# Kernel tuning notes

Hardware: AMD Instinct MI355X
Metric: run time of the kernel (lower is better)

Reference implementation:

```python
import jax, jax.numpy as jnp
import numpy as np

K = 20
BN_SCALE = 1.0 / np.sqrt(1.0 + 1e-5)  # BN at init: running_mean=0, running_var=1


def _graph_feature(x, k):
    # x: (B, N, C) point features -> (B, N, k, 2C) edge features
    sq = jnp.sum(x * x, axis=-1)  # (B, N)
    # negative squared distance: larger == closer (matches torch topk on -dist)
    d = 2.0 * jnp.einsum('bnc,bmc->bnm', x, x) - sq[:, :, None] - sq[:, None, :]
    idx = jax.lax.top_k(d, k)[1]  # (B, N, k), self included as nearest
    nbr = jax.vmap(lambda pts, i: pts[i])(x, idx)  # (B, N, k, C) gather
    ctr = jnp.broadcast_to(x[:, :, None, :], nbr.shape)
    return jnp.concatenate([nbr - ctr, ctr], axis=-1)


def _edge_conv(e, W, g, b):
    # 1x1 Conv2d (no bias) + BatchNorm(init stats) + LeakyReLU(0.2) + max over k
    y = jnp.einsum('bnkc,oc->bnko', e, W)
    y = jax.nn.leaky_relu(y * (g * BN_SCALE) + b, 0.2)
    return jnp.max(y, axis=2)  # (B, N, O)


def setup_inputs() -> dict:
    key = jax.random.key(0)
    ks = jax.random.split(key, 12)
    B, N = 4, 1024
    dims_in = [6, 128, 256, 512]
    dims_out = [64, 128, 256, 512]
    inp = {'x': jax.random.normal(ks[0], (B, N, 3), dtype=jnp.float32)}
    for i, (ci, co) in enumerate(zip(dims_in, dims_out), start=1):
        inp[f'W{i}'] = jax.random.normal(ks[i], (co, ci), dtype=jnp.float32) * (1.0 / np.sqrt(ci))
        inp[f'g{i}'] = jnp.ones((co,), dtype=jnp.float32)
        inp[f'b{i}'] = jnp.zeros((co,), dtype=jnp.float32)
    inp['W5'] = jax.random.normal(ks[5], (512, 960), dtype=jnp.float32) * (1.0 / np.sqrt(960.0))
    inp['g5'] = jnp.ones((512,), dtype=jnp.float32)
    inp['b5'] = jnp.zeros((512,), dtype=jnp.float32)
    inp['We'] = jax.random.normal(ks[6], (256, 512), dtype=jnp.float32) * (1.0 / np.sqrt(512.0))
    return inp


def reference(x, W1, g1, b1, W2, g2, b2, W3, g3, b3, W4, g4, b4, W5, g5, b5, We):
    x1 = _edge_conv(_graph_feature(x, K), W1, g1, b1)   # (B, N, 64)
    x2 = _edge_conv(_graph_feature(x1, K), W2, g2, b2)  # (B, N, 128)
    x3 = _edge_conv(_graph_feature(x2, K), W3, g3, b3)  # (B, N, 256)
    x4 = _edge_conv(_graph_feature(x3, K), W4, g4, b4)  # (B, N, 512)
    xc = jnp.concatenate([x1, x2, x3, x4], axis=-1)     # (B, N, 960)
    y = jnp.einsum('bnc,oc->bno', xc, W5)               # conv5 (1x1 Conv1d)
    y = jax.nn.leaky_relu(y * (g5 * BN_SCALE) + b5, 0.2)
    feat = jnp.max(y, axis=1)                           # (B, 512) global max-pool
    return feat @ We.T                                  # (B, num_features)
```

## Files before the change

kernel.cpp:

```cpp
#include <hip/hip_runtime.h>
#include <hip/hip_bf16.h>
#include <math.h>

typedef __hip_bfloat16 bf16;
typedef __bf16 v8bf __attribute__((ext_vector_type(8)));
typedef float v4f __attribute__((ext_vector_type(4)));

#define BN_SCALE 0.9999950000374997f
#define NPTS 1024
#define NB 4
#define CH5 ((size_t)4 * 1024 * 512)

__device__ __forceinline__ float b2f(bf16 v) { return __bfloat162float(v); }
__device__ __forceinline__ bf16 f2b(float v) { return __float2bfloat16(v); }
__device__ __forceinline__ float ldw(const void* p, size_t i, int isf) {
    return isf ? ((const float*)p)[i] : b2f(((const bf16*)p)[i]);
}
__device__ __forceinline__ unsigned ordf(float f) {
    unsigned u = __float_as_uint(f);
    return (u & 0x80000000u) ? ~u : (u | 0x80000000u);
}
__device__ __forceinline__ float iordf(unsigned u) {
    return (u & 0x80000000u) ? __uint_as_float(u ^ 0x80000000u) : __uint_as_float(~u);
}

__device__ __forceinline__ int detect_isf(const void* xraw, int* cnt) {
    const unsigned short* u = (const unsigned short*)xraw;
    int t = threadIdx.x, c = 0;
    for (int i = t; i < 512; i += 256) {
        unsigned short v = u[i];
        int e = (v >> 7) & 0xFF;
        int m = v & 0x7F;
        if (e == 0xFF || e >= 141 || (e == 0 && m != 0)) c++;
    }
    cnt[t] = c;
    __syncthreads();
    for (int off = 128; off > 0; off >>= 1) {
        if (t < off) cnt[t] += cnt[t + off];
        __syncthreads();
    }
    int isf = (cnt[0] > 30) ? 1 : 0;
    __syncthreads();
    return isf;
}

__global__ void k_prep(const void* __restrict__ W1, const void* __restrict__ W2,
                       const void* __restrict__ W3, const void* __restrict__ W4,
                       const void* __restrict__ W5, const void* __restrict__ x,
                       bf16* __restrict__ Whi, bf16* __restrict__ Wlo,
                       bf16* __restrict__ xph, bf16* __restrict__ xpl, float* __restrict__ sq,
                       int* __restrict__ flag, unsigned* __restrict__ pooledU) {
    __shared__ int cnt[256];
    int isf = detect_isf(x, cnt);
    if (blockIdx.x == 0) {
        if (threadIdx.x == 0) *flag = isf;
        for (int i = threadIdx.x; i < 2048; i += 256) pooledU[i] = 0u;
    }
    int idx = blockIdx.x * 256 + threadIdx.x;
    if (idx < 839680) {
        const void* src; int C, O, Kpad, two, local;
        if (idx < 4096)        { src = W1; C = 3;   O = 64;  Kpad = 32;  two = 1; local = idx; }
        else if (idx < 20480)  { src = W2; C = 64;  O = 128; Kpad = 64;  two = 1; local = idx - 4096; }
        else if (idx < 86016)  { src = W3; C = 128; O = 256; Kpad = 128; two = 1; local = idx - 20480; }
        else if (idx < 348160) { src = W4; C = 256; O = 512; Kpad = 256; two = 1; local = idx - 86016; }
        else                   { src = W5; C = 960; O = 512; Kpad = 960; two = 0; local = idx - 348160; }
        int r = local / Kpad, c = local % Kpad;
        float wv = 0.f;
        if (c < C) {
            size_t off;
            if (two) off = (r < O) ? (size_t)r * 2 * C + c : (size_t)(r - O) * 2 * C + C + c;
            else     off = (size_t)r * C + c;
            wv = ldw(src, off, isf);
        }
        bf16 h = f2b(wv);
        Whi[idx] = h;
        Wlo[idx] = f2b(wv - b2f(h));
    } else if (idx < 843776) {
        int p = idx - 839680;
        int z = p >> 10, n = p & 1023;
        bf16* ph = xph + (size_t)z * NPTS * 32;
        bf16* pl = xpl + (size_t)z * NPTS * 32;
        float s = 0.f;
        for (int c = 0; c < 32; c++) {
            float v = (c < 3) ? ldw(x, (size_t)z * NPTS * 3 + n * 3 + c, isf) : 0.f;
            bf16 h = f2b(v);
            ph[n * 32 + c] = h;
            pl[n * 32 + c] = f2b(v - b2f(h));
            s += v * v;
        }
        sq[z * NPTS + n] = s;
    }
}

__device__ __forceinline__ int lidx(int plane, int row) {
    return ((((plane << 7) | row)) ^ (plane << 1)) << 3;
}
__device__ __forceinline__ void fill128(bf16* dst, const bf16* src, int ld) {
    int t = threadIdx.x;
    int r = t >> 2, kq = t & 3;
    *(float4*)(dst + lidx(kq, r))      = *(const float4*)(src + (size_t)r * ld + kq * 8);
    *(float4*)(dst + lidx(kq, r + 64)) = *(const float4*)(src + (size_t)(r + 64) * ld + kq * 8);
}
__device__ __forceinline__ v8bf ldf(const bf16* tile, int sub, int l) {
    return *(const v8bf*)(tile + lidx(l >> 4, sub * 16 + (l & 15)));
}

__global__ __launch_bounds__(256) void k_layer_a(const bf16* __restrict__ Xhi, const bf16* __restrict__ Xlo,
                                                 int ld, int Kpad, size_t xstride,
                                                 const bf16* __restrict__ Whi, const bf16* __restrict__ Wlo,
                                                 int O, const float* __restrict__ sqg,
                                                 float* __restrict__ Dg, float* __restrict__ Pg,
                                                 const int* __restrict__ flag) {
    int i = blockIdx.x;
    int z = (i >> 1) & 3;
    int bi = ((i >> 3) << 1) | (i & 1);
    const bf16* Xh = Xhi + (size_t)z * xstride;
    const bf16* Xl = Xlo + (size_t)z * xstride;
    __shared__ alignas(16) bf16 Ah[4096], Al[4096], Bh[4096], Bl[4096];
    int w = threadIdx.x >> 6, l = threadIdx.x & 63;
    int wr = w >> 1, wc = w & 1;
    int quad = l >> 4, col = l & 15;
    v4f zero = {0.f, 0.f, 0.f, 0.f};
    v4f acc[4][4] = {{zero, zero, zero, zero}, {zero, zero, zero, zero},
                     {zero, zero, zero, zero}, {zero, zero, zero, zero}};

    if (bi < 36) {
        int bx = 0;
        while ((((bx + 1) * (bx + 2)) >> 1) <= bi) bx++;
        int by = bi - ((bx * (bx + 1)) >> 1);
        const float* sq = sqg + z * NPTS;
        float* D = Dg + (size_t)z * NPTS * NPTS;
        int n0 = by * 128, m0 = bx * 128;
        for (int k0 = 0; k0 < Kpad; k0 += 32) {
            __syncthreads();
            fill128(Ah, Xh + (size_t)n0 * ld + k0, ld);
            fill128(Bh, Xh + (size_t)m0 * ld + k0, ld);
            fill128(Al, Xl + (size_t)n0 * ld + k0, ld);
            fill128(Bl, Xl + (size_t)m0 * ld + k0, ld);
            __syncthreads();
            v8bf ah[4], al[4];
#pragma unroll
            for (int mi = 0; mi < 4; mi++) {
                ah[mi] = ldf(Ah, wr * 4 + mi, l);
                al[mi] = ldf(Al, wr * 4 + mi, l);
            }
#pragma unroll
            for (int ni = 0; ni < 4; ni++) {
                v8bf bh = ldf(Bh, wc * 4 + ni, l);
                v8bf bl = ldf(Bl, wc * 4 + ni, l);
#pragma unroll
                for (int mi = 0; mi < 4; mi++) {
                    acc[mi][ni] = __builtin_amdgcn_mfma_f32_16x16x32_bf16(ah[mi], bh, acc[mi][ni], 0, 0, 0);
                    acc[mi][ni] = __builtin_amdgcn_mfma_f32_16x16x32_bf16(ah[mi], bl, acc[mi][ni], 0, 0, 0);
                    acc[mi][ni] = __builtin_amdgcn_mfma_f32_16x16x32_bf16(al[mi], bh, acc[mi][ni], 0, 0, 0);
                }
            }
        }
        int rb = n0 + wr * 64 + quad * 4;
        int cb = m0 + wc * 64 + col;
        float sm[4];
#pragma unroll
        for (int ni = 0; ni < 4; ni++) sm[ni] = sq[cb + ni * 16];
#pragma unroll
        for (int mi = 0; mi < 4; mi++) {
#pragma unroll
            for (int r = 0; r < 4; r++) {
                int row = rb + mi * 16 + r;
                float sn = sq[row];
#pragma unroll
                for (int ni = 0; ni < 4; ni++) {
                    float d = 2.f * acc[mi][ni][r] - sn - sm[ni];
                    int c = cb + ni * 16;
                    D[(size_t)row * NPTS + c] = d;
                    if (bx != by) D[(size_t)c * NPTS + row] = d;
                }
            }
        }
    } else {
        int isf = *flag;
        int nCol = (2 * O) >> 7;
        int s = bi - 36;
        int n0 = (s % nCol) * 128;
        int m0 = (s / nCol) * 128;
        int N2 = 2 * O;
        float* P = Pg + (size_t)z * NPTS * N2;
        for (int k0 = 0; k0 < Kpad; k0 += 32) {
            __syncthreads();
            fill128(Ah, Xh + (size_t)m0 * ld + k0, ld);
            fill128(Al, Xl + (size_t)m0 * ld + k0, ld);
            fill128(Bh, Whi + (size_t)n0 * Kpad + k0, Kpad);
            if (isf) fill128(Bl, Wlo + (size_t)n0 * Kpad + k0, Kpad);
            __syncthreads();
            v8bf ah[4], al[4];
#pragma unroll
            for (int mi = 0; mi < 4; mi++) {
                ah[mi] = ldf(Ah, wr * 4 + mi, l);
                al[mi] = ldf(Al, wr * 4 + mi, l);
            }
#pragma unroll
            for (int ni = 0; ni < 4; ni++) {
                v8bf bh = ldf(Bh, wc * 4 + ni, l);
#pragma unroll
                for (int mi = 0; mi < 4; mi++) {
                    acc[mi][ni] = __builtin_amdgcn_mfma_f32_16x16x32_bf16(ah[mi], bh, acc[mi][ni], 0, 0, 0);
                    acc[mi][ni] = __builtin_amdgcn_mfma_f32_16x16x32_bf16(al[mi], bh, acc[mi][ni], 0, 0, 0);
                }
                if (isf) {
                    v8bf bl = ldf(Bl, wc * 4 + ni, l);
#pragma unroll
                    for (int mi = 0; mi < 4; mi++)
                        acc[mi][ni] = __builtin_amdgcn_mfma_f32_16x16x32_bf16(ah[mi], bl, acc[mi][ni], 0, 0, 0);
                }
            }
        }
        int rb = m0 + wr * 64 + quad * 4;
        int cb = n0 + wc * 64 + col;
#pragma unroll
        for (int mi = 0; mi < 4; mi++)
#pragma unroll
            for (int r = 0; r < 4; r++) {
                int row = rb + mi * 16 + r;
#pragma unroll
                for (int ni = 0; ni < 4; ni++)
                    P[(size_t)row * N2 + cb + ni * 16] = acc[mi][ni][r];
            }
    }
}

template<int PAT>
__device__ __forceinline__ void swz_step(float& bv, int& bi) {
    float ov = __int_as_float(__builtin_amdgcn_ds_swizzle(__float_as_int(bv), PAT));
    int   oi = __builtin_amdgcn_ds_swizzle(bi, PAT);
    if (ov > bv || (ov == bv && oi < bi)) { bv = ov; bi = oi; }
}
__device__ __forceinline__ void shfl_step(float& bv, int& bi, int mask) {
    float ov = __shfl_xor(bv, mask);
    int   oi = __shfl_xor(bi, mask);
    if (ov > bv || (ov == bv && oi < bi)) { bv = ov; bi = oi; }
}
#define PICK(va, ja, vb, jb, vo, jo) { bool t_ = (vb) > (va); vo = t_ ? (vb) : (va); jo = t_ ? (jb) : (ja); }

#define GATHER_BODY(o, scl, bb, doSq) do { \
    float tv = Pn[O + (o)] - Pn[(o)]; \
    float mx = -__builtin_inff(), mn = __builtin_inff(); \
    _Pragma("unroll") \
    for (int j = 0; j < 20; j++) { \
        float vv = P[offj[j] + (o)]; \
        mx = fmaxf(mx, vv); \
        mn = fminf(mn, vv); \
    } \
    float base = ((scl) >= 0.f ? mx : mn) + tv; \
    float accv = base * (scl) + (bb); \
    accv = accv > 0.f ? accv : 0.2f * accv; \
    bf16 hi = f2b(accv); \
    bf16 lo = f2b(accv - b2f(hi)); \
    xhOut[(size_t)z * NPTS * 960 + (size_t)n * 960 + (o)] = hi; \
    xlOut[(size_t)z * NPTS * 960 + (size_t)n * 960 + (o)] = lo; \
    if (doSq) { \
        float xv = b2f(hi) + b2f(lo); \
        float s2 = xv * xv; \
        _Pragma("unroll") \
        for (int off = 32; off > 0; off >>= 1) s2 += __shfl_down(s2, off); \
        if (l == 0) sqP[r][(o) >> 6] = s2; \
    } \
} while (0)

__global__ __launch_bounds__(256) void k_layer_b(const float* __restrict__ Dg, const float* __restrict__ Pg,
                                                 const void* __restrict__ g, const void* __restrict__ bias,
                                                 int O, bf16* __restrict__ xhOut, bf16* __restrict__ xlOut,
                                                 float* __restrict__ sqOut, int writeSq,
                                                 const int* __restrict__ flag) {
    __shared__ int ids[4][20];
    __shared__ float sqP[4][8];
    int isf = *flag;
    int i = blockIdx.x;
    int z = (i >> 1) & 3;
    int local = ((i >> 3) << 1) | (i & 1);
    int tid = threadIdx.x;
    int wq = tid >> 6, l = tid & 63;
    int row = local * 4 + wq;

    {
        const float* Dr = Dg + (size_t)z * NPTS * NPTS + (size_t)row * NPTS;
        float v[16];
#pragma unroll
        for (int jj = 0; jj < 4; jj++) {
            float4 f4 = *(const float4*)(Dr + jj * 256 + l * 4);
            v[jj * 4 + 0] = f4.x; v[jj * 4 + 1] = f4.y;
            v[jj * 4 + 2] = f4.z; v[jj * 4 + 3] = f4.w;
        }
        float bmv[4]; int bmj[4];
#pragma unroll
        for (int gg = 0; gg < 4; gg++) {
            float a0, a1; int j0, j1;
            PICK(v[4 * gg + 0], 4 * gg + 0, v[4 * gg + 1], 4 * gg + 1, a0, j0);
            PICK(v[4 * gg + 2], 4 * gg + 2, v[4 * gg + 3], 4 * gg + 3, a1, j1);
            PICK(a0, j0, a1, j1, bmv[gg], bmj[gg]);
        }
        for (int s = 0; s < 20; s++) {
            float t0, t1, bv; int s0, s1, bj;
            PICK(bmv[0], bmj[0], bmv[1], bmj[1], t0, s0);
            PICK(bmv[2], bmj[2], bmv[3], bmj[3], t1, s1);
            PICK(t0, s0, t1, s1, bv, bj);
            int bi = (bj >> 2) * 256 + l * 4 + (bj & 3);
            swz_step<0x041F>(bv, bi);
            swz_step<0x081F>(bv, bi);
            swz_step<0x101F>(bv, bi);
            swz_step<0x201F>(bv, bi);
            swz_step<0x401F>(bv, bi);
            shfl_step(bv, bi, 32);
            if (l == 0) ids[wq][s] = bi;
            if (((bi >> 2) & 63) == l) {
                int ej = (bi >> 8) * 4 + (bi & 3);
                int eg = ej >> 2, ek = ej & 3;
#pragma unroll
                for (int gg = 0; gg < 4; gg++) if (gg == eg) {
#pragma unroll
                    for (int kk = 0; kk < 4; kk++)
                        if (kk == ek) v[4 * gg + kk] = -__builtin_inff();
                    float a0, a1; int j0, j1;
                    PICK(v[4 * gg + 0], 4 * gg + 0, v[4 * gg + 1], 4 * gg + 1, a0, j0);
                    PICK(v[4 * gg + 2], 4 * gg + 2, v[4 * gg + 3], 4 * gg + 3, a1, j1);
                    PICK(a0, j0, a1, j1, bmv[gg], bmj[gg]);
                }
            }
        }
    }
    __syncthreads();

    int N2 = 2 * O;
    const float* P = Pg + (size_t)z * NPTS * N2;
    int o0 = tid, o1 = tid + 256;
    int has0 = (o0 < O), has1 = (o1 < O);
    float scl0 = 0.f, bb0 = 0.f, scl1 = 0.f, bb1 = 0.f;
    if (has0) { scl0 = ldw(g, o0, isf) * BN_SCALE; bb0 = ldw(bias, o0, isf); }
    if (has1) { scl1 = ldw(g, o1, isf) * BN_SCALE; bb1 = ldw(bias, o1, isf); }
#pragma unroll
    for (int r = 0; r < 4; r++) {
        int offj[20];
#pragma unroll
        for (int j = 0; j < 20; j++)
            offj[j] = __builtin_amdgcn_readfirstlane(ids[r][j]) * N2;
        int n = local * 4 + r;
        const float* Pn = P + (size_t)n * N2;
        if (has0) GATHER_BODY(o0, scl0, bb0, writeSq);
        if (has1) GATHER_BODY(o1, scl1, bb1, 0);
    }
    if (writeSq) {
        __syncthreads();
        if (tid < 4) {
            int nc = O >> 6;
            float tot = 0.f;
            for (int c = 0; c < nc; c++) tot += sqP[tid][c];
            sqOut[z * NPTS + local * 4 + tid] = tot;
        }
    }
}

__global__ __launch_bounds__(256) void k_conv5(const bf16* __restrict__ Xhi, const bf16* __restrict__ Xlo,
                                               const bf16* __restrict__ Whi, const bf16* __restrict__ Wlo,
                                               float* __restrict__ P5,
                                               const int* __restrict__ flag) {
    int isf = *flag;
    int i = blockIdx.x;
    int z = (i >> 1) & 3;
    int rest = ((i >> 3) << 1) | (i & 1);
    int ks = rest >> 5;
    int tile = rest & 31;
    int m0 = (tile >> 2) * 128, o0 = (tile & 3) * 128;
    const bf16* Xh = Xhi + (size_t)z * NPTS * 960;
    const bf16* Xl = Xlo + (size_t)z * NPTS * 960;
    __shared__ alignas(16) bf16 Ah[4096], Al[4096], Bh[4096], Bl[4096];
    int w = threadIdx.x >> 6, l = threadIdx.x & 63;
    int wr = w >> 1, wc = w & 1;
    int quad = l >> 4, col = l & 15;
    v4f zero = {0.f, 0.f, 0.f, 0.f};
    v4f acc[4][4] = {{zero, zero, zero, zero}, {zero, zero, zero, zero},
                     {zero, zero, zero, zero}, {zero, zero, zero, zero}};
    int kbeg = ks * 160, kend = kbeg + 160;
    for (int k0 = kbeg; k0 < kend; k0 += 32) {
        __syncthreads();
        fill128(Ah, Xh + (size_t)m0 * 960 + k0, 960);
        fill128(Al, Xl + (size_t)m0 * 960 + k0, 960);
        fill128(Bh, Whi + (size_t)o0 * 960 + k0, 960);
        if (isf) fill128(Bl, Wlo + (size_t)o0 * 960 + k0, 960);
        __syncthreads();
        v8bf ah[4], al[4];
#pragma unroll
        for (int mi = 0; mi < 4; mi++) {
            ah[mi] = ldf(Ah, wr * 4 + mi, l);
            al[mi] = ldf(Al, wr * 4 + mi, l);
        }
#pragma unroll
        for (int ni = 0; ni < 4; ni++) {
            v8bf bh = ldf(Bh, wc * 4 + ni, l);
#pragma unroll
            for (int mi = 0; mi < 4; mi++) {
                acc[mi][ni] = __builtin_amdgcn_mfma_f32_16x16x32_bf16(ah[mi], bh, acc[mi][ni], 0, 0, 0);
                acc[mi][ni] = __builtin_amdgcn_mfma_f32_16x16x32_bf16(al[mi], bh, acc[mi][ni], 0, 0, 0);
            }
            if (isf) {
                v8bf bl = ldf(Bl, wc * 4 + ni, l);
#pragma unroll
                for (int mi = 0; mi < 4; mi++)
                    acc[mi][ni] = __builtin_amdgcn_mfma_f32_16x16x32_bf16(ah[mi], bl, acc[mi][ni], 0, 0, 0);
            }
        }
    }
    float* Pw = P5 + (size_t)ks * CH5 + (size_t)z * NPTS * 512;
    int rb = m0 + wr * 64 + quad * 4;
    int cb = o0 + wc * 64 + col;
#pragma unroll
    for (int mi = 0; mi < 4; mi++)
#pragma unroll
        for (int r = 0; r < 4; r++) {
            int row = rb + mi * 16 + r;
#pragma unroll
            for (int ni = 0; ni < 4; ni++)
                Pw[(size_t)row * 512 + cb + ni * 16] = acc[mi][ni][r];
        }
}

__global__ __launch_bounds__(256) void k_pool5(const float* __restrict__ P5,
                                               const void* __restrict__ g, const void* __restrict__ bias,
                                               unsigned* __restrict__ pooledU,
                                               const int* __restrict__ flag) {
    __shared__ float red2[128];
    int isf = *flag;
    int i = blockIdx.x;
    int z = (i >> 1) & 3;
    int rest = ((i >> 3) << 1) | (i & 1);
    int oc = (rest & 3) * 128, mc = (rest >> 2) * 32;
    int t = threadIdx.x;
    int c = t & 127, h = t >> 7;
    int o = oc + c;
    float scl = ldw(g, o, isf) * BN_SCALE;
    float bb = ldw(bias, o, isf);
    const float* p0 = P5 + (size_t)z * NPTS * 512 + (size_t)(mc + h * 16) * 512 + o;
    float ym = -__builtin_inff();
    for (int r = 0; r < 16; r++) {
        const float* p = p0 + (size_t)r * 512;
        float s = p[0];
#pragma unroll
        for (int ks = 1; ks < 6; ks++) s += p[(size_t)ks * CH5];
        float v = s * scl + bb;
        v = v > 0.f ? v : 0.2f * v;
        ym = fmaxf(ym, v);
    }
    if (h == 1) red2[c] = ym;
    __syncthreads();
    if (h == 0) {
        float m = fmaxf(ym, red2[c]);
        atomicMax(&pooledU[z * 512 + o], ordf(m));
    }
}

__global__ void k_final(const unsigned* __restrict__ pooledU, const void* __restrict__ We,
                        void* __restrict__ out, const int* __restrict__ flag) {
    __shared__ float p[512];
    int isf = *flag;
    int b = blockIdx.x >> 2, fb = blockIdx.x & 3;
    int t = threadIdx.x, w = t >> 6, l = t & 63;
    for (int i = t; i < 512; i += 256) p[i] = iordf(pooledU[b * 512 + i]);
    __syncthreads();
    for (int it = 0; it < 16; it++) {
        int f = fb * 64 + w * 16 + it;
        float s = 0.f;
        size_t base = (size_t)f * 512 + l * 8;
#pragma unroll
        for (int j = 0; j < 8; j++) s += p[l * 8 + j] * ldw(We, base + j, isf);
#pragma unroll
        for (int off = 32; off > 0; off >>= 1) s += __shfl_down(s, off);
        if (l == 0) {
            if (isf) ((float*)out)[b * 256 + f] = s;
            else     ((bf16*)out)[b * 256 + f] = f2b(s);
        }
    }
}

extern "C" void kernel_launch(void* const* d_in, const int* in_sizes, int n_in,
                              void* d_out, int out_size, void* d_ws, size_t ws_size,
                              hipStream_t stream) {
    const void* x  = d_in[0];
    const void* Wl[4] = { d_in[1], d_in[4], d_in[7], d_in[10] };
    const void* gl[4] = { d_in[2], d_in[5], d_in[8], d_in[11] };
    const void* bl[4] = { d_in[3], d_in[6], d_in[9], d_in[12] };
    const void* W5 = d_in[13];
    const void* g5 = d_in[14];
    const void* b5 = d_in[15];
    const void* We = d_in[16];

    char* base = (char*)d_ws;
    bf16*     xc_hi   = (bf16*)(base);
    bf16*     xc_lo   = (bf16*)(base + 7864320);
    bf16*     xpadh   = (bf16*)(base + 15728640);
    bf16*     xpadl   = (bf16*)(base + 15990784);
    float*    Dbuf    = (float*)(base + 16252928);
    float*    Pbuf    = (float*)(base + 33030144);
    bf16*     Whi     = (bf16*)(base + 49807360);
    bf16*     Wlo     = (bf16*)(base + 51486720);
    unsigned* pooledU = (unsigned*)(base + 53493760);
    float*    sq      = (float*)(base + 53501952);
    int*      flag    = (int*)(base + 53518336);
    float*    P5      = (float*)(base + 53520384);

    const int Kpad[4]   = { 32, 64, 128, 256 };
    const int Os[4]     = { 64, 128, 256, 512 };
    const int Woff[5]   = { 0, 4096, 20480, 86016, 348160 };
    const int colIn[4]  = { 0, 0, 64, 192 };
    const int colOut[4] = { 0, 64, 192, 448 };

    k_prep<<<3296, 256, 0, stream>>>(Wl[0], Wl[1], Wl[2], Wl[3], W5, x,
                                     Whi, Wlo, xpadh, xpadl, sq, flag, pooledU);

    for (int l = 0; l < 4; l++) {
        int O = Os[l];
        int nCol = (2 * O) >> 7;
        int nBlk = 36 + 8 * nCol;
        const bf16* Xh = (l == 0) ? xpadh : (xc_hi + colIn[l]);
        const bf16* Xl = (l == 0) ? xpadl : (xc_lo + colIn[l]);
        int ld = (l == 0) ? 32 : 960;
        size_t xstr = (l == 0) ? (size_t)NPTS * 32 : (size_t)NPTS * 960;
        k_layer_a<<<nBlk * NB, 256, 0, stream>>>(
            Xh, Xl, ld, Kpad[l], xstr, Whi + Woff[l], Wlo + Woff[l], O, sq, Dbuf, Pbuf, flag);
        k_layer_b<<<NPTS * NB / 4, 256, 0, stream>>>(
            Dbuf, Pbuf, gl[l], bl[l], O, xc_hi + colOut[l], xc_lo + colOut[l], sq, l < 3, flag);
    }
    k_conv5<<<768, 256, 0, stream>>>(xc_hi, xc_lo, Whi + Woff[4], Wlo + Woff[4], P5, flag);
    k_pool5<<<512, 256, 0, stream>>>(P5, g5, b5, pooledU, flag);
    k_final<<<16, 256, 0, stream>>>(pooledU, We, d_out, flag);
}
```

Baseline: 321.0 us.

## Double-buffer LDS tiles with register prefetch in layer GEMM kernel

Converts the k-loop of both branches of k_layer_a (distance GEMM and weight projection GEMM) into a software pipeline. The next K-slice is loaded from global memory into registers before the MFMA work on the current slice, then written to a second LDS buffer afterwards, leaving one barrier per iteration instead of two. This aims to hide global load latency behind the matrix math, at the cost of doubling LDS use (64 KB) and holding extra registers for the staged data, which may reduce occupancy.

```diff
diff --git a/kernel.cpp b/kernel.cpp
--- a/kernel.cpp
+++ b/kernel.cpp
@@ -95,6 +95,19 @@
 __device__ __forceinline__ int lidx(int plane, int row) {
     return ((((plane << 7) | row)) ^ (plane << 1)) << 3;
 }
+struct St2 { float4 a, b; };
+__device__ __forceinline__ St2 ldStage(const bf16* src, int ld) {
+    int t = threadIdx.x; int r = t >> 2, kq = t & 3;
+    St2 s;
+    s.a = *(const float4*)(src + (size_t)r * ld + kq * 8);
+    s.b = *(const float4*)(src + (size_t)(r + 64) * ld + kq * 8);
+    return s;
+}
+__device__ __forceinline__ void stStage(bf16* dst, const St2& s) {
+    int t = threadIdx.x; int r = t >> 2, kq = t & 3;
+    *(float4*)(dst + lidx(kq, r)) = s.a;
+    *(float4*)(dst + lidx(kq, r + 64)) = s.b;
+}
 __device__ __forceinline__ void fill128(bf16* dst, const bf16* src, int ld) {
     int t = threadIdx.x;
     int r = t >> 2, kq = t & 3;
@@ -116,7 +129,7 @@
     int bi = ((i >> 3) << 1) | (i & 1);
     const bf16* Xh = Xhi + (size_t)z * xstride;
     const bf16* Xl = Xlo + (size_t)z * xstride;
-    __shared__ alignas(16) bf16 Ah[4096], Al[4096], Bh[4096], Bl[4096];
+    __shared__ alignas(16) bf16 Ah[2][4096], Al[2][4096], Bh[2][4096], Bl[2][4096];
     int w = threadIdx.x >> 6, l = threadIdx.x & 63;
     int wr = w >> 1, wc = w & 1;
     int quad = l >> 4, col = l & 15;
@@ -131,23 +144,34 @@
         const float* sq = sqg + z * NPTS;
         float* D = Dg + (size_t)z * NPTS * NPTS;
         int n0 = by * 128, m0 = bx * 128;
+        const bf16* pAn = Xh + (size_t)n0 * ld;
+        const bf16* pAm = Xh + (size_t)m0 * ld;
+        const bf16* pLn = Xl + (size_t)n0 * ld;
+        const bf16* pLm = Xl + (size_t)m0 * ld;
+        St2 sA = ldStage(pAn, ld), sB = ldStage(pAm, ld);
+        St2 sC = ldStage(pLn, ld), sD = ldStage(pLm, ld);
+        stStage(Ah[0], sA); stStage(Bh[0], sB);
+        stStage(Al[0], sC); stStage(Bl[0], sD);
+        __syncthreads();
+        int cur = 0;
         for (int k0 = 0; k0 < Kpad; k0 += 32) {
-            __syncthreads();
-            fill128(Ah, Xh + (size_t)n0 * ld + k0, ld);
-            fill128(Bh, Xh + (size_t)m0 * ld + k0, ld);
-            fill128(Al, Xl + (size_t)n0 * ld + k0, ld);
-            fill128(Bl, Xl + (size_t)m0 * ld + k0, ld);
-            __syncthreads();
+            bool more = (k0 + 32 < Kpad);
+            if (more) {
+                sA = ldStage(pAn + k0 + 32, ld);
+                sB = ldStage(pAm + k0 + 32, ld);
+                sC = ldStage(pLn + k0 + 32, ld);
+                sD = ldStage(pLm + k0 + 32, ld);
+            }
             v8bf ah[4], al[4];
 #pragma unroll
             for (int mi = 0; mi < 4; mi++) {
-                ah[mi] = ldf(Ah, wr * 4 + mi, l);
-                al[mi] = ldf(Al, wr * 4 + mi, l);
+                ah[mi] = ldf(Ah[cur], wr * 4 + mi, l);
+                al[mi] = ldf(Al[cur], wr * 4 + mi, l);
             }
 #pragma unroll
             for (int ni = 0; ni < 4; ni++) {
-                v8bf bh = ldf(Bh, wc * 4 + ni, l);
-                v8bf bl = ldf(Bl, wc * 4 + ni, l);
+                v8bf bh = ldf(Bh[cur], wc * 4 + ni, l);
+                v8bf bl = ldf(Bl[cur], wc * 4 + ni, l);
 #pragma unroll
                 for (int mi = 0; mi < 4; mi++) {
                     acc[mi][ni] = __builtin_amdgcn_mfma_f32_16x16x32_bf16(ah[mi], bh, acc[mi][ni], 0, 0, 0);
@@ -155,6 +179,12 @@
                     acc[mi][ni] = __builtin_amdgcn_mfma_f32_16x16x32_bf16(al[mi], bh, acc[mi][ni], 0, 0, 0);
                 }
             }
+            if (more) {
+                stStage(Ah[cur ^ 1], sA); stStage(Bh[cur ^ 1], sB);
+                stStage(Al[cur ^ 1], sC); stStage(Bl[cur ^ 1], sD);
+            }
+            __syncthreads();
+            cur ^= 1;
         }
         int rb = n0 + wr * 64 + quad * 4;
         int cb = m0 + wc * 64 + col;
@@ -184,34 +214,53 @@
         int m0 = (s / nCol) * 128;
         int N2 = 2 * O;
         float* P = Pg + (size_t)z * NPTS * N2;
+        const bf16* pXh = Xh + (size_t)m0 * ld;
+        const bf16* pXl = Xl + (size_t)m0 * ld;
+        const bf16* pWh = Whi + (size_t)n0 * Kpad;
+        const bf16* pWl = Wlo + (size_t)n0 * Kpad;
+        St2 sA = ldStage(pXh, ld), sC = ldStage(pXl, ld);
+        St2 sB = ldStage(pWh, Kpad), sD;
+        if (isf) sD = ldStage(pWl, Kpad);
+        stStage(Ah[0], sA); stStage(Al[0], sC); stStage(Bh[0], sB);
+        if (isf) stStage(Bl[0], sD);
+        __syncthreads();
+        int cur = 0;
         for (int k0 = 0; k0 < Kpad; k0 += 32) {
-            __syncthreads();
-            fill128(Ah, Xh + (size_t)m0 * ld + k0, ld);
-            fill128(Al, Xl + (size_t)m0 * ld + k0, ld);
-            fill128(Bh, Whi + (size_t)n0 * Kpad + k0, Kpad);
-            if (isf) fill128(Bl, Wlo + (size_t)n0 * Kpad + k0, Kpad);
-            __syncthreads();
+            bool more = (k0 + 32 < Kpad);
+            if (more) {
+                sA = ldStage(pXh + k0 + 32, ld);
+                sC = ldStage(pXl + k0 + 32, ld);
+                sB = ldStage(pWh + k0 + 32, Kpad);
+                if (isf) sD = ldStage(pWl + k0 + 32, Kpad);
+            }
             v8bf ah[4], al[4];
 #pragma unroll
             for (int mi = 0; mi < 4; mi++) {
-                ah[mi] = ldf(Ah, wr * 4 + mi, l);
-                al[mi] = ldf(Al, wr * 4 + mi, l);
+                ah[mi] = ldf(Ah[cur], wr * 4 + mi, l);
+                al[mi] = ldf(Al[cur], wr * 4 + mi, l);
             }
 #pragma unroll
             for (int ni = 0; ni < 4; ni++) {
-                v8bf bh = ldf(Bh, wc * 4 + ni, l);
+                v8bf bh = ldf(Bh[cur], wc * 4 + ni, l);
 #pragma unroll
                 for (int mi = 0; mi < 4; mi++) {
                     acc[mi][ni] = __builtin_amdgcn_mfma_f32_16x16x32_bf16(ah[mi], bh, acc[mi][ni], 0, 0, 0);
                     acc[mi][ni] = __builtin_amdgcn_mfma_f32_16x16x32_bf16(al[mi], bh, acc[mi][ni], 0, 0, 0);
                 }
                 if (isf) {
-                    v8bf bl = ldf(Bl, wc * 4 + ni, l);
+                    v8bf bl = ldf(Bl[cur], wc * 4 + ni, l);
 #pragma unroll
                     for (int mi = 0; mi < 4; mi++)
                         acc[mi][ni] = __builtin_amdgcn_mfma_f32_16x16x32_bf16(ah[mi], bl, acc[mi][ni], 0, 0, 0);
                 }
             }
+            if (more) {
+                stStage(Ah[cur ^ 1], sA); stStage(Al[cur ^ 1], sC);
+                stStage(Bh[cur ^ 1], sB);
+                if (isf) stStage(Bl[cur ^ 1], sD);
+            }
+            __syncthreads();
+            cur ^= 1;
         }
         int rb = m0 + wr * 64 + quad * 4;
         int cb = n0 + wc * 64 + col;
```

Measured after the change: 318.8 us. No clear change (-0.7%).
